# Performance work log

Hardware: AMD Instinct MI355X
Metric: run time of the kernel (lower is better)

The kernel has to match this reference:

```python
import jax, jax.numpy as jnp
import numpy as np

B, TQ, TK, D, H = 4, 2048, 2048, 512, 8
NEG = -1e9
LN_EPS = 1e-3  # Keras LayerNormalization default


def setup_inputs() -> dict:
    key = jax.random.key(0)
    ks = jax.random.split(key, 5)
    s = 0.02
    return {
        "queries": jax.random.normal(ks[0], (B, TQ, D), jnp.float32),
        "keys_in": jax.random.normal(ks[1], (B, TK, D), jnp.float32),
        "Wq": jax.random.normal(ks[2], (D, D), jnp.float32) * s,
        "bq": jnp.zeros((D,), jnp.float32),
        "Wk": jax.random.normal(ks[3], (D, D), jnp.float32) * s,
        "bk": jnp.zeros((D,), jnp.float32),
        "Wv": jax.random.normal(ks[4], (D, D), jnp.float32) * s,
        "bv": jnp.zeros((D,), jnp.float32),
        "gamma": jnp.ones((D,), jnp.float32),
        "beta": jnp.zeros((D,), jnp.float32),
    }


def reference(queries, keys_in, Wq, bq, Wk, bk, Wv, bv, gamma, beta):
    # Dense projections with relu activation (as in the original layer)
    Q = jax.nn.relu(queries @ Wq + bq)   # [B, Tq, D]
    K = jax.nn.relu(keys_in @ Wk + bk)   # [B, Tk, D]
    V = jax.nn.relu(keys_in @ Wv + bv)   # [B, Tk, D]

    b, tq, d = Q.shape
    tk = K.shape[1]
    dh = d // H
    # split_heads: tf.split(axis=-1)+concat(axis=0) == contiguous feature chunks per head
    Qh = Q.reshape(b, tq, H, dh)
    Kh = K.reshape(b, tk, H, dh)
    Vh = V.reshape(b, tk, H, dh)

    scores = jnp.einsum('bqhd,bkhd->bhqk', Qh, Kh) / jnp.sqrt(jnp.float32(dh))

    # key padding mask derived from per-head K content: sum(|K|) > 0 along dh
    kmask = jnp.sum(jnp.abs(Kh), axis=-1) > 0            # [B, Tk, H]
    kmask = jnp.transpose(kmask, (0, 2, 1))              # [B, H, Tk]
    scores = jnp.where(kmask[:, :, None, :], scores, NEG)

    attn = jax.nn.softmax(scores, axis=-1)               # [B, H, Tq, Tk]

    # query mask: zero out attention rows for all-zero query positions
    qmask = (jnp.sum(jnp.abs(Qh), axis=-1) > 0).astype(attn.dtype)  # [B, Tq, H]
    qmask = jnp.transpose(qmask, (0, 2, 1))              # [B, H, Tq]
    attn = attn * qmask[:, :, :, None]

    out = jnp.einsum('bhqk,bkhd->bqhd', attn, Vh).reshape(b, tq, d)

    # residual + LayerNorm (Keras default: last axis, eps=1e-3)
    res = out + queries
    mu = jnp.mean(res, axis=-1, keepdims=True)
    var = jnp.var(res, axis=-1, keepdims=True)
    return (res - mu) * jax.lax.rsqrt(var + LN_EPS) * gamma + beta
```

## Files before the change

### kernel.cpp

```cpp
#include <hip/hip_runtime.h>
#include <cstdint>

#define BB 4
#define TT 2048
#define DD 512
#define HH 8
#define DH 64
#define NT (TT / 64)
#define LOG2E 1.4426950408889634f

using bf16x8 = __attribute__((ext_vector_type(8))) __bf16;
using f32x4  = __attribute__((ext_vector_type(4))) float;
using f32x16 = __attribute__((ext_vector_type(16))) float;
using us8    = __attribute__((ext_vector_type(8))) unsigned short;
using us4    = __attribute__((ext_vector_type(4))) unsigned short;
using u32x2  = __attribute__((ext_vector_type(2))) unsigned int;

typedef const __attribute__((address_space(1))) unsigned int* as1cp;
typedef __attribute__((address_space(3))) unsigned int* as3p;

__device__ __forceinline__ void gload16(const void* g, void* l) {
  __builtin_amdgcn_global_load_lds((as1cp)(uintptr_t)g,
                                   (as3p)(unsigned int)(uintptr_t)l, 16, 0, 0);
}

__device__ __forceinline__ unsigned short f2bf(float x) {
  unsigned int u = __float_as_uint(x);
  u += 0x7fffu + ((u >> 16) & 1u);
  return (unsigned short)(u >> 16);
}
__device__ __forceinline__ float bf2f(unsigned short u) {
  return __uint_as_float(((unsigned int)u) << 16);
}
__device__ __forceinline__ f32x4 MFMA(bf16x8 a, bf16x8 b, f32x4 c) {
  return __builtin_amdgcn_mfma_f32_16x16x32_bf16(a, b, c, 0, 0, 0);
}
__device__ __forceinline__ f32x16 MFMA32(bf16x8 a, bf16x8 b, f32x16 c) {
  return __builtin_amdgcn_mfma_f32_32x32x16_bf16(a, b, c, 0, 0, 0);
}

#define WAITVM(N) asm volatile("s_waitcnt vmcnt(" #N ")" ::: "memory")
#define RAWBAR() asm volatile("s_barrier" ::: "memory")

__global__ __launch_bounds__(256) void prep_kernel(const float4* __restrict__ q,
                                                   const float4* __restrict__ k,
                                                   us4* __restrict__ qb,
                                                   us4* __restrict__ kb,
                                                   const float* __restrict__ Wq,
                                                   const float* __restrict__ Wk,
                                                   const float* __restrict__ Wv,
                                                   unsigned short* __restrict__ Wt) {
  __shared__ float tile[32][33];
  int id = blockIdx.x;
  if (id < 4096) {
    size_t i = (size_t)id * 256 + threadIdx.x;
    float4 a = q[i];
    us4 o; o[0] = f2bf(a.x); o[1] = f2bf(a.y); o[2] = f2bf(a.z); o[3] = f2bf(a.w);
    qb[i] = o;
    float4 b = k[i];
    us4 p; p[0] = f2bf(b.x); p[1] = f2bf(b.y); p[2] = f2bf(b.z); p[3] = f2bf(b.w);
    kb[i] = p;
  } else {
    int id2 = id - 4096;
    int z = id2 >> 8, rem = id2 & 255;
    const float* W = (z == 0) ? Wq : (z == 1) ? Wk : Wv;
    int k0 = (rem & 15) * 32, n0 = (rem >> 4) * 32;
    int r = threadIdx.x >> 5, c = threadIdx.x & 31;
#pragma unroll
    for (int p = 0; p < 4; ++p)
      tile[r + p * 8][c] = W[(size_t)(k0 + r + p * 8) * DD + n0 + c];
    __syncthreads();
    unsigned short* o = Wt + (size_t)z * DD * DD;
#pragma unroll
    for (int p = 0; p < 4; ++p)
      o[(size_t)(n0 + r + p * 8) * DD + k0 + c] = f2bf(tile[c][r + p * 8]);
  }
}

#define GSTAGE(kt2, pbuf)                                                    \
  {                                                                          \
    int t_ = threadIdx.x;                                                    \
    _Pragma("unroll")                                                        \
    for (int it_ = 0; it_ < 2; ++it_) {                                      \
      int c_ = t_ + it_ * 256;                                               \
      gload16(A  + (size_t)(mb + (c_ >> 2)) * DD + (kt2) * 32 + (c_ & 3) * 8,\
              &As[pbuf][(size_t)c_ * 8]);                                    \
      gload16(Bt + (size_t)(nb + (c_ >> 2)) * DD + (kt2) * 32 + (c_ & 3) * 8,\
              &Bs[pbuf][(size_t)c_ * 8]);                                    \
    }                                                                        \
  }

__global__ __launch_bounds__(256) void gemm_proj(const unsigned short* __restrict__ qb,
                                                 const unsigned short* __restrict__ kb,
                                                 const unsigned short* __restrict__ Wt,
                                                 const float* __restrict__ bq,
                                                 const float* __restrict__ bk,
                                                 const float* __restrict__ bv,
                                                 unsigned short* __restrict__ Qp,
                                                 unsigned short* __restrict__ Kp,
                                                 unsigned short* __restrict__ Vp) {
  int z = blockIdx.z;
  const unsigned short* A  = (z == 0) ? qb : kb;
  const unsigned short* Bt = Wt + (size_t)z * DD * DD;
  const float* bias = (z == 0) ? bq : (z == 1) ? bk : bv;
  unsigned short* out = (z == 0) ? Qp : (z == 1) ? Kp : Vp;
  const float osc = (z == 0) ? 0.125f * LOG2E : 1.0f;

  __shared__ __align__(16) unsigned short As[2][128 * 32];
  __shared__ __align__(16) unsigned short Bs[2][128 * 32];

  int mb = blockIdx.x * 128, nb = blockIdx.y * 128;
  int w = threadIdx.x >> 6, lane = threadIdx.x & 63;
  int l15 = lane & 15, lg = lane >> 4;
  int wr = (w >> 1) * 64, wc = (w & 1) * 64;

  f32x4 acc[4][4] = {};

  GSTAGE(0, 0);
  for (int kt = 0; kt < DD / 32; ++kt) {
    int pb2 = kt & 1;
    if (kt + 1 < DD / 32) {
      GSTAGE(kt + 1, pb2 ^ 1);
      WAITVM(4);
    } else {
      WAITVM(0);
    }
    RAWBAR();

    bf16x8 af[4], bf[4];
#pragma unroll
    for (int m = 0; m < 4; ++m)
      af[m] = *(const bf16x8*)&As[pb2][(wr + m * 16 + l15) * 32 + lg * 8];
#pragma unroll
    for (int n = 0; n < 4; ++n)
      bf[n] = *(const bf16x8*)&Bs[pb2][(wc + n * 16 + l15) * 32 + lg * 8];
#pragma unroll
    for (int m = 0; m < 4; ++m)
#pragma unroll
      for (int n = 0; n < 4; ++n)
        acc[m][n] = MFMA(af[m], bf[n], acc[m][n]);

    if (kt + 1 < DD / 32) RAWBAR();
  }

#pragma unroll
  for (int m = 0; m < 4; ++m)
#pragma unroll
    for (int n = 0; n < 4; ++n)
#pragma unroll
      for (int i = 0; i < 4; ++i) {
        int row = mb + wr + m * 16 + lg * 4 + i;
        int col = nb + wc + n * 16 + l15;
        float v = acc[m][n][i] + bias[col];
        out[(size_t)row * DD + col] = f2bf(fmaxf(v, 0.f) * osc);
      }
}

__global__ __launch_bounds__(256) void post_proj(const unsigned short* __restrict__ Qp,
                                                 const unsigned short* __restrict__ Kp,
                                                 const unsigned short* __restrict__ Vp,
                                                 unsigned short* __restrict__ Vt,
                                                 float* __restrict__ qmask,
                                                 uint2* __restrict__ kbits) {
  __shared__ unsigned short tile[64][72];
  int id = blockIdx.x;
  if (id < 1024) {
    int b = id >> 8, k0 = (id & 31) * 64, d0 = ((id >> 5) & 7) * 64;
    int t = threadIdx.x;
    int r = t >> 3, c8 = (t & 7) * 8;
#pragma unroll
    for (int p = 0; p < 2; ++p) {
      int row = r + p * 32;
      us8 v = *(const us8*)&Vp[(size_t)(b * TT + k0 + row) * DD + d0 + c8];
#pragma unroll
      for (int j = 0; j < 8; ++j) tile[row][c8 + j] = v[j];
    }
    __syncthreads();
#pragma unroll
    for (int p = 0; p < 2; ++p) {
      int dr = r + p * 32;
      us8 o;
#pragma unroll
      for (int j = 0; j < 8; ++j) o[j] = tile[c8 + j][dr];
      *(us8*)&Vt[((size_t)b * DD + d0 + dr) * TT + k0 + c8] = o;
    }
  } else {
    int wid = (id - 1024) * 4 + (threadIdx.x >> 6);
    int lane = threadIdx.x & 63;
    int side = wid >> 10;
    int rem = wid & 1023;
    int bh = rem >> 5, tl = rem & 31;
    int b = bh >> 3, h = bh & 7;
    const unsigned short* src =
        (side ? Kp : Qp) + ((size_t)(b * TT + tl * 64 + lane)) * DD + h * DH;
    float s = 0.f;
#pragma unroll
    for (int j = 0; j < 64; j += 8) {
      us8 v = *(const us8*)(src + j);
#pragma unroll
      for (int e = 0; e < 8; ++e) s += bf2f(v[e]);
    }
    if (side == 0) {
      qmask[(size_t)bh * TT + tl * 64 + lane] = (s > 0.f) ? 1.f : 0.f;
    } else {
      unsigned long long mb = __ballot(s > 0.f);
      if (lane == 0)
        kbits[bh * NT + tl] = make_uint2((unsigned int)mb, (unsigned int)(mb >> 32));
    }
  }
}

#define STAGE(tt, pbuf)                                                      \
  {                                                                          \
    int c0_ = threadIdx.x;                                                   \
    _Pragma("unroll")                                                        \
    for (int it_ = 0; it_ < 2; ++it_) {                                      \
      int c_ = c0_ + it_ * 256;                                              \
      int r_ = c_ >> 3, j_ = c_ & 7;                                         \
      int js_ = j_ ^ (r_ & 7);                                               \
      int kr_ = (r_ & ~12) | ((r_ & 4) << 1) | ((r_ & 8) >> 1);              \
      gload16(kg + (size_t)((tt) * 64 + kr_) * DD + js_ * 8,                 \
              &KsBuf[pbuf][(size_t)c_ * 8]);                                 \
      gload16(vg + (size_t)r_ * TT + (tt) * 64 + js_ * 8,                    \
              &VsBuf[pbuf][(size_t)c_ * 8]);                                 \
    }                                                                        \
  }

__global__ __launch_bounds__(256) void attn_kernel(
    const unsigned short* __restrict__ Qp,
    const unsigned short* __restrict__ Kp,
    const unsigned short* __restrict__ Vt,
    const uint2* __restrict__ kbits,
    const float* __restrict__ qmask,
    float* __restrict__ O) {
  __shared__ __align__(16) unsigned short KsBuf[2][64 * 64];
  __shared__ __align__(16) unsigned short VsBuf[2][64 * 64];

  const int w = threadIdx.x >> 6;
  const int lane = threadIdx.x & 63;
  const int l31 = lane & 31, h2 = lane >> 5;

  int flat = blockIdx.x;
  int wg = (flat & 7) * 64 + (flat >> 3);
  int qt = wg & 15, bh = wg >> 4;
  int h = bh & 7, b = bh >> 3;
  int q0 = qt * 128 + w * 32;

  const unsigned short* qbase =
      Qp + ((size_t)(b * TT + q0 + l31)) * DD + h * DH + h2 * 8;
  bf16x8 qf[4];
#pragma unroll
  for (int kd = 0; kd < 4; ++kd) qf[kd] = *(const bf16x8*)(qbase + kd * 16);

  const unsigned short* kg = Kp + ((size_t)b * TT) * DD + h * DH;
  const unsigned short* vg = Vt + ((size_t)(b * DD + h * DH)) * TT;
  const uint2* kb_ptr = kbits + (size_t)bh * NT;

  f32x16 oat0 = {}, oat1 = {};
  float m_i = -1e30f, l_i = 0.f;

  STAGE(0, 0);

  for (int t = 0; t < NT; ++t) {
    int pb = t & 1;
    if (t + 1 < NT) {
      STAGE(t + 1, pb ^ 1);
      WAITVM(4);
    } else {
      WAITVM(0);
    }
    RAWBAR();

    const unsigned short* ksb = &KsBuf[pb][0];
    const unsigned short* vsb = &VsBuf[pb][0];

    bf16x8 kf0[4], kf1[4], vf0[4], vf1[4];
#pragma unroll
    for (int kd = 0; kd < 4; ++kd) {
      int x = ((kd * 2 + h2) ^ (l31 & 7)) << 3;
      kf0[kd] = *(const bf16x8*)&ksb[l31 * 64 + x];
      kf1[kd] = *(const bf16x8*)&ksb[(32 + l31) * 64 + x];
      vf0[kd] = *(const bf16x8*)&vsb[l31 * 64 + x];
      vf1[kd] = *(const bf16x8*)&vsb[(32 + l31) * 64 + x];
    }

    f32x16 s0 = {}, s1 = {};
    __builtin_amdgcn_s_setprio(1);
#pragma unroll
    for (int kd = 0; kd < 4; ++kd) s0 = MFMA32(kf0[kd], qf[kd], s0);
#pragma unroll
    for (int kd = 0; kd < 4; ++kd) s1 = MFMA32(kf1[kd], qf[kd], s1);
    __builtin_amdgcn_s_setprio(0);

    uint2 kw = kb_ptr[t];
    if ((kw.x & kw.y) != 0xffffffffu) {
#pragma unroll
      for (int r = 0; r < 16; ++r) {
        int sh = ((r >> 3) << 4) + (h2 << 3) + (r & 7);
        if (!((kw.x >> sh) & 1)) s0[r] = -1e30f;
        if (!((kw.y >> sh) & 1)) s1[r] = -1e30f;
      }
    }

    float x0 = fmaxf(fmaxf(fmaxf(s0[0], s0[1]), fmaxf(s0[2], s0[3])),
                     fmaxf(fmaxf(s0[4], s0[5]), fmaxf(s0[6], s0[7])));
    float x1 = fmaxf(fmaxf(fmaxf(s0[8], s0[9]), fmaxf(s0[10], s0[11])),
                     fmaxf(fmaxf(s0[12], s0[13]), fmaxf(s0[14], s0[15])));
    float x2 = fmaxf(fmaxf(fmaxf(s1[0], s1[1]), fmaxf(s1[2], s1[3])),
                     fmaxf(fmaxf(s1[4], s1[5]), fmaxf(s1[6], s1[7])));
    float x3 = fmaxf(fmaxf(fmaxf(s1[8], s1[9]), fmaxf(s1[10], s1[11])),
                     fmaxf(fmaxf(s1[12], s1[13]), fmaxf(s1[14], s1[15])));
    float pm = fmaxf(fmaxf(x0, x1), fmaxf(x2, x3));
    u32x2 sw = __builtin_amdgcn_permlane32_swap(__float_as_uint(pm),
                                                __float_as_uint(pm), false, false);
    pm = fmaxf(__uint_as_float(sw[0]), __uint_as_float(sw[1]));

    if (__any(pm > m_i + 12.f)) {
      float mn = fmaxf(m_i, pm);
      float al = exp2f(m_i - mn);
      m_i = mn;
      l_i *= al;
#pragma unroll
      for (int r = 0; r < 16; ++r) { oat0[r] *= al; oat1[r] *= al; }
    }

    float a0 = 0.f, a1 = 0.f, a2 = 0.f, a3 = 0.f;
#pragma unroll
    for (int r = 0; r < 8; ++r)  { float p = exp2f(s0[r] - m_i); s0[r] = p; a0 += p; }
#pragma unroll
    for (int r = 8; r < 16; ++r) { float p = exp2f(s0[r] - m_i); s0[r] = p; a1 += p; }
#pragma unroll
    for (int r = 0; r < 8; ++r)  { float p = exp2f(s1[r] - m_i); s1[r] = p; a2 += p; }
#pragma unroll
    for (int r = 8; r < 16; ++r) { float p = exp2f(s1[r] - m_i); s1[r] = p; a3 += p; }
    float rs = (a0 + a1) + (a2 + a3);
    u32x2 sr = __builtin_amdgcn_permlane32_swap(__float_as_uint(rs),
                                                __float_as_uint(rs), false, false);
    rs = __uint_as_float(sr[0]) + __uint_as_float(sr[1]);
    l_i += rs;

    bf16x8 pbf[4];
#pragma unroll
    for (int j = 0; j < 8; ++j) {
      pbf[0][j] = (__bf16)s0[j];
      pbf[1][j] = (__bf16)s0[8 + j];
      pbf[2][j] = (__bf16)s1[j];
      pbf[3][j] = (__bf16)s1[8 + j];
    }

    __builtin_amdgcn_s_setprio(1);
#pragma unroll
    for (int ks = 0; ks < 4; ++ks) {
      oat0 = MFMA32(vf0[ks], pbf[ks], oat0);
      oat1 = MFMA32(vf1[ks], pbf[ks], oat1);
    }
    __builtin_amdgcn_s_setprio(0);

    if (t + 1 < NT) RAWBAR();
  }

  float qm = qmask[(size_t)bh * TT + q0 + l31];
  float sc = qm / fmaxf(l_i, 1e-30f);
  float* ob = O + ((size_t)(b * TT + q0 + l31)) * DD + h * DH + h2 * 4;
#pragma unroll
  for (int qq = 0; qq < 4; ++qq) {
    float4 v0 = make_float4(oat0[4 * qq + 0] * sc, oat0[4 * qq + 1] * sc,
                            oat0[4 * qq + 2] * sc, oat0[4 * qq + 3] * sc);
    *(float4*)(ob + 8 * qq) = v0;
    float4 v1 = make_float4(oat1[4 * qq + 0] * sc, oat1[4 * qq + 1] * sc,
                            oat1[4 * qq + 2] * sc, oat1[4 * qq + 3] * sc);
    *(float4*)(ob + 32 + 8 * qq) = v1;
  }
}

__global__ __launch_bounds__(256) void ln_kernel(const float* __restrict__ O,
                                                 const float* __restrict__ qin,
                                                 const float* __restrict__ gamma,
                                                 const float* __restrict__ beta,
                                                 float* __restrict__ out) {
  int row = blockIdx.x * 4 + (threadIdx.x >> 6);
  int lane = threadIdx.x & 63;
  size_t base = (size_t)row * DD + lane * 8;
  const float4* o4 = (const float4*)(O + base);
  const float4* q4 = (const float4*)(qin + base);
  float4 a = o4[0], b2 = o4[1], c = q4[0], d2 = q4[1];
  float v[8];
  v[0] = a.x + c.x; v[1] = a.y + c.y; v[2] = a.z + c.z; v[3] = a.w + c.w;
  v[4] = b2.x + d2.x; v[5] = b2.y + d2.y; v[6] = b2.z + d2.z; v[7] = b2.w + d2.w;
  float s = 0.f, s2 = 0.f;
#pragma unroll
  for (int j = 0; j < 8; ++j) { s += v[j]; s2 += v[j] * v[j]; }
#pragma unroll
  for (int xm = 1; xm < 64; xm <<= 1) {
    s += __shfl_xor(s, xm);
    s2 += __shfl_xor(s2, xm);
  }
  float mu = s * (1.0f / DD);
  float var = s2 * (1.0f / DD) - mu * mu;
  float rs = rsqrtf(var + 1e-3f);
  const float* g = gamma + lane * 8;
  const float* bb = beta + lane * 8;
  float* ob = out + base;
#pragma unroll
  for (int j = 0; j < 8; ++j) ob[j] = (v[j] - mu) * rs * g[j] + bb[j];
}

extern "C" void kernel_launch(void* const* d_in, const int* in_sizes, int n_in,
                              void* d_out, int out_size, void* d_ws, size_t ws_size,
                              hipStream_t stream) {
  (void)in_sizes; (void)n_in; (void)out_size; (void)ws_size;
  const float* queries = (const float*)d_in[0];
  const float* keys_in = (const float*)d_in[1];
  const float* Wq = (const float*)d_in[2];
  const float* bq = (const float*)d_in[3];
  const float* Wk = (const float*)d_in[4];
  const float* bk = (const float*)d_in[5];
  const float* Wv = (const float*)d_in[6];
  const float* bv = (const float*)d_in[7];
  const float* gamma = (const float*)d_in[8];
  const float* beta  = (const float*)d_in[9];
  float* out = (float*)d_out;

  char* ws = (char*)d_ws;
  unsigned short* qb = (unsigned short*)(ws);
  unsigned short* kb = (unsigned short*)(ws + (8ull << 20));
  float*          O  = (float*)(ws);
  unsigned short* Qp = (unsigned short*)(ws + (16ull << 20));
  unsigned short* Kp = (unsigned short*)(ws + (24ull << 20));
  unsigned short* Vp = (unsigned short*)(ws + (32ull << 20));
  unsigned short* Vt = (unsigned short*)(ws + (40ull << 20));
  unsigned short* Wt = (unsigned short*)(ws + (48ull << 20));
  float* qmaskp = (float*)(ws + (50ull << 20));
  uint2* kbitsp = (uint2*)(ws + (50ull << 20) + (512ull << 10));

  prep_kernel<<<4864, 256, 0, stream>>>((const float4*)queries, (const float4*)keys_in,
                                        (us4*)qb, (us4*)kb, Wq, Wk, Wv, Wt);
  gemm_proj<<<dim3(64, 4, 3), 256, 0, stream>>>(qb, kb, Wt, bq, bk, bv, Qp, Kp, Vp);
  post_proj<<<1536, 256, 0, stream>>>(Qp, Kp, Vp, Vt, qmaskp, kbitsp);
  attn_kernel<<<512, 256, 0, stream>>>(Qp, Kp, Vt, kbitsp, qmaskp, O);
  ln_kernel<<<2048, 256, 0, stream>>>(O, queries, gamma, beta, out);
}
```

Before: 203.0 us.

## Pre-pack K/V into MFMA fragment order and load directly to registers

post_proj now writes K and V into per-tile layouts that already match the MFMA operand fragments. This lets the attention kernel drop its LDS staging, barriers and async global-to-LDS copies, and instead software-pipeline K fragments in registers with coalesced 16-byte global loads. The attention output is also stored as bf16 rather than fp32, which shrinks the write and the LayerNorm read. In exchange, the four waves in a block no longer share K/V through LDS, so each wave fetches its own copy from global memory or L2. The bf16 output also loses precision before the residual add.

```diff
diff --git a/kernel.cpp b/kernel.cpp
--- a/kernel.cpp
+++ b/kernel.cpp
@@ -159,34 +159,52 @@
 __global__ __launch_bounds__(256) void post_proj(const unsigned short* __restrict__ Qp,
                                                  const unsigned short* __restrict__ Kp,
                                                  const unsigned short* __restrict__ Vp,
-                                                 unsigned short* __restrict__ Vt,
+                                                 unsigned short* __restrict__ Kpack,
+                                                 unsigned short* __restrict__ Vpack,
                                                  float* __restrict__ qmask,
                                                  uint2* __restrict__ kbits) {
-  __shared__ unsigned short tile[64][72];
+  __shared__ __align__(16) unsigned short tile[64 * 256];
   int id = blockIdx.x;
-  if (id < 1024) {
-    int b = id >> 8, k0 = (id & 31) * 64, d0 = ((id >> 5) & 7) * 64;
-    int t = threadIdx.x;
-    int r = t >> 3, c8 = (t & 7) * 8;
-#pragma unroll
-    for (int p = 0; p < 2; ++p) {
-      int row = r + p * 32;
-      us8 v = *(const us8*)&Vp[(size_t)(b * TT + k0 + row) * DD + d0 + c8];
-#pragma unroll
-      for (int j = 0; j < 8; ++j) tile[row][c8 + j] = v[j];
+  int w = threadIdx.x >> 6, lane = threadIdx.x & 63;
+  int l31 = lane & 31, h2 = lane >> 5;
+
+  if (id < 256) {
+    int b = id >> 6, t = (id >> 1) & 31, hg = id & 1;
+    {
+      int c0 = threadIdx.x;
+#pragma unroll
+      for (int it = 0; it < 8; ++it) {
+        int c = c0 + it * 256;
+        int row = c >> 5, ch = c & 31;
+        gload16(Vp + ((size_t)(b * TT + t * 64 + row)) * DD + hg * 256 + ch * 8,
+                tile + (size_t)c * 8);
+      }
     }
     __syncthreads();
 #pragma unroll
-    for (int p = 0; p < 2; ++p) {
-      int dr = r + p * 32;
+    for (int cc = 0; cc < 8; ++cc) {
+      int chunk = w * 8 + cc;
+      int hh = chunk >> 3, half = (cc >> 2) & 1, ks = cc & 3;
       us8 o;
 #pragma unroll
-      for (int j = 0; j < 8; ++j) o[j] = tile[c8 + j][dr];
-      *(us8*)&Vt[((size_t)b * DD + d0 + dr) * TT + k0 + c8] = o;
-    }
+      for (int j = 0; j < 8; ++j)
+        o[j] = tile[(ks * 16 + h2 * 8 + j) * 256 + hh * 64 + half * 32 + l31];
+      int bh = b * 8 + hg * 4 + hh;
+      *(us8*)(Vpack + ((((size_t)bh * NT + t) * 2 + half) * 4 + ks) * 512 + lane * 8) = o;
+    }
+  } else if (id < 768) {
+    int wid = (id - 256) * 4 + w;
+    int n = wid & 1, t = (wid >> 1) & 31, bh = wid >> 6;
+    int b = bh >> 3, h = bh & 7;
+    int bs = (l31 & ~12) | ((l31 & 4) << 1) | ((l31 & 8) >> 1);
+    const unsigned short* src =
+        Kp + ((size_t)(b * TT + t * 64 + 32 * n + bs)) * DD + h * DH + h2 * 8;
+    unsigned short* dst = Kpack + (((size_t)bh * NT + t) * 2 + n) * 2048 + lane * 8;
+#pragma unroll
+    for (int kd = 0; kd < 4; ++kd)
+      *(us8*)(dst + kd * 512) = *(const us8*)(src + kd * 16);
   } else {
-    int wid = (id - 1024) * 4 + (threadIdx.x >> 6);
-    int lane = threadIdx.x & 63;
+    int wid = (id - 768) * 4 + w;
     int side = wid >> 10;
     int rem = wid & 1023;
     int bh = rem >> 5, tl = rem & 31;
@@ -210,32 +228,101 @@
   }
 }
 
-#define STAGE(tt, pbuf)                                                      \
-  {                                                                          \
-    int c0_ = threadIdx.x;                                                   \
-    _Pragma("unroll")                                                        \
-    for (int it_ = 0; it_ < 2; ++it_) {                                      \
-      int c_ = c0_ + it_ * 256;                                              \
-      int r_ = c_ >> 3, j_ = c_ & 7;                                         \
-      int js_ = j_ ^ (r_ & 7);                                               \
-      int kr_ = (r_ & ~12) | ((r_ & 4) << 1) | ((r_ & 8) >> 1);              \
-      gload16(kg + (size_t)((tt) * 64 + kr_) * DD + js_ * 8,                 \
-              &KsBuf[pbuf][(size_t)c_ * 8]);                                 \
-      gload16(vg + (size_t)r_ * TT + (tt) * 64 + js_ * 8,                    \
-              &VsBuf[pbuf][(size_t)c_ * 8]);                                 \
-    }                                                                        \
-  }
+__device__ __forceinline__ void attn_body(
+    int t, int tp,
+    const bf16x8 (&Kc)[8], bf16x8 (&Kn)[8], const bf16x8 (&qf)[4],
+    f32x16& oat0, f32x16& oat1, float& m_i, float& l_i,
+    const unsigned short* __restrict__ kgp, const unsigned short* __restrict__ vgp,
+    const uint2* __restrict__ kb_ptr, int h2) {
+  f32x16 s0 = {}, s1 = {};
+  __builtin_amdgcn_s_setprio(1);
+#pragma unroll
+  for (int kd = 0; kd < 4; ++kd) s0 = MFMA32(Kc[kd], qf[kd], s0);
+#pragma unroll
+  for (int kd = 0; kd < 4; ++kd) s1 = MFMA32(Kc[4 + kd], qf[kd], s1);
+  __builtin_amdgcn_s_setprio(0);
+
+  const unsigned short* kn = kgp + (size_t)tp * 4096;
+#pragma unroll
+  for (int c = 0; c < 8; ++c) Kn[c] = *(const bf16x8*)(kn + c * 512);
+
+  bf16x8 vc[8];
+  const unsigned short* vp = vgp + (size_t)t * 4096;
+#pragma unroll
+  for (int c = 0; c < 8; ++c) vc[c] = *(const bf16x8*)(vp + c * 512);
+
+  uint2 kw = kb_ptr[t];
+  if ((kw.x & kw.y) != 0xffffffffu) {
+#pragma unroll
+    for (int r = 0; r < 16; ++r) {
+      int sh = ((r >> 3) << 4) + (h2 << 3) + (r & 7);
+      if (!((kw.x >> sh) & 1)) s0[r] = -1e30f;
+      if (!((kw.y >> sh) & 1)) s1[r] = -1e30f;
+    }
+  }
+
+  float x0 = fmaxf(fmaxf(fmaxf(s0[0], s0[1]), fmaxf(s0[2], s0[3])),
+                   fmaxf(fmaxf(s0[4], s0[5]), fmaxf(s0[6], s0[7])));
+  float x1 = fmaxf(fmaxf(fmaxf(s0[8], s0[9]), fmaxf(s0[10], s0[11])),
+                   fmaxf(fmaxf(s0[12], s0[13]), fmaxf(s0[14], s0[15])));
+  float x2 = fmaxf(fmaxf(fmaxf(s1[0], s1[1]), fmaxf(s1[2], s1[3])),
+                   fmaxf(fmaxf(s1[4], s1[5]), fmaxf(s1[6], s1[7])));
+  float x3 = fmaxf(fmaxf(fmaxf(s1[8], s1[9]), fmaxf(s1[10], s1[11])),
+                   fmaxf(fmaxf(s1[12], s1[13]), fmaxf(s1[14], s1[15])));
+  float pm = fmaxf(fmaxf(x0, x1), fmaxf(x2, x3));
+  u32x2 sw = __builtin_amdgcn_permlane32_swap(__float_as_uint(pm),
+                                              __float_as_uint(pm), false, false);
+  pm = fmaxf(__uint_as_float(sw[0]), __uint_as_float(sw[1]));
+
+  if (__any(pm > m_i + 12.f)) {
+    float mn = fmaxf(m_i, pm);
+    float al = exp2f(m_i - mn);
+    m_i = mn;
+    l_i *= al;
+#pragma unroll
+    for (int r = 0; r < 16; ++r) { oat0[r] *= al; oat1[r] *= al; }
+  }
+
+  float a0 = 0.f, a1 = 0.f, a2 = 0.f, a3 = 0.f;
+#pragma unroll
+  for (int r = 0; r < 8; ++r)  { float p = exp2f(s0[r] - m_i); s0[r] = p; a0 += p; }
+#pragma unroll
+  for (int r = 8; r < 16; ++r) { float p = exp2f(s0[r] - m_i); s0[r] = p; a1 += p; }
+#pragma unroll
+  for (int r = 0; r < 8; ++r)  { float p = exp2f(s1[r] - m_i); s1[r] = p; a2 += p; }
+#pragma unroll
+  for (int r = 8; r < 16; ++r) { float p = exp2f(s1[r] - m_i); s1[r] = p; a3 += p; }
+  float rs = (a0 + a1) + (a2 + a3);
+  u32x2 sr = __builtin_amdgcn_permlane32_swap(__float_as_uint(rs),
+                                              __float_as_uint(rs), false, false);
+  rs = __uint_as_float(sr[0]) + __uint_as_float(sr[1]);
+  l_i += rs;
+
+  bf16x8 pbf[4];
+#pragma unroll
+  for (int j = 0; j < 8; ++j) {
+    pbf[0][j] = (__bf16)s0[j];
+    pbf[1][j] = (__bf16)s0[8 + j];
+    pbf[2][j] = (__bf16)s1[j];
+    pbf[3][j] = (__bf16)s1[8 + j];
+  }
+
+  __builtin_amdgcn_s_setprio(1);
+#pragma unroll
+  for (int ks = 0; ks < 4; ++ks) {
+    oat0 = MFMA32(vc[ks], pbf[ks], oat0);
+    oat1 = MFMA32(vc[4 + ks], pbf[ks], oat1);
+  }
+  __builtin_amdgcn_s_setprio(0);
+}
 
 __global__ __launch_bounds__(256) void attn_kernel(
     const unsigned short* __restrict__ Qp,
-    const unsigned short* __restrict__ Kp,
-    const unsigned short* __restrict__ Vt,
+    const unsigned short* __restrict__ Kpack,
+    const unsigned short* __restrict__ Vpack,
     const uint2* __restrict__ kbits,
     const float* __restrict__ qmask,
-    float* __restrict__ O) {
-  __shared__ __align__(16) unsigned short KsBuf[2][64 * 64];
-  __shared__ __align__(16) unsigned short VsBuf[2][64 * 64];
-
+    unsigned short* __restrict__ O) {
   const int w = threadIdx.x >> 6;
   const int lane = threadIdx.x & 63;
   const int l31 = lane & 31, h2 = lane >> 5;
@@ -252,128 +339,40 @@
 #pragma unroll
   for (int kd = 0; kd < 4; ++kd) qf[kd] = *(const bf16x8*)(qbase + kd * 16);
 
-  const unsigned short* kg = Kp + ((size_t)b * TT) * DD + h * DH;
-  const unsigned short* vg = Vt + ((size_t)(b * DD + h * DH)) * TT;
+  const unsigned short* kgp = Kpack + (size_t)bh * NT * 4096 + lane * 8;
+  const unsigned short* vgp = Vpack + (size_t)bh * NT * 4096 + lane * 8;
   const uint2* kb_ptr = kbits + (size_t)bh * NT;
 
   f32x16 oat0 = {}, oat1 = {};
   float m_i = -1e30f, l_i = 0.f;
 
-  STAGE(0, 0);
-
-  for (int t = 0; t < NT; ++t) {
-    int pb = t & 1;
-    if (t + 1 < NT) {
-      STAGE(t + 1, pb ^ 1);
-      WAITVM(4);
-    } else {
-      WAITVM(0);
-    }
-    RAWBAR();
-
-    const unsigned short* ksb = &KsBuf[pb][0];
-    const unsigned short* vsb = &VsBuf[pb][0];
-
-    bf16x8 kf0[4], kf1[4], vf0[4], vf1[4];
-#pragma unroll
-    for (int kd = 0; kd < 4; ++kd) {
-      int x = ((kd * 2 + h2) ^ (l31 & 7)) << 3;
-      kf0[kd] = *(const bf16x8*)&ksb[l31 * 64 + x];
-      kf1[kd] = *(const bf16x8*)&ksb[(32 + l31) * 64 + x];
-      vf0[kd] = *(const bf16x8*)&vsb[l31 * 64 + x];
-      vf1[kd] = *(const bf16x8*)&vsb[(32 + l31) * 64 + x];
-    }
-
-    f32x16 s0 = {}, s1 = {};
-    __builtin_amdgcn_s_setprio(1);
-#pragma unroll
-    for (int kd = 0; kd < 4; ++kd) s0 = MFMA32(kf0[kd], qf[kd], s0);
-#pragma unroll
-    for (int kd = 0; kd < 4; ++kd) s1 = MFMA32(kf1[kd], qf[kd], s1);
-    __builtin_amdgcn_s_setprio(0);
-
-    uint2 kw = kb_ptr[t];
-    if ((kw.x & kw.y) != 0xffffffffu) {
-#pragma unroll
-      for (int r = 0; r < 16; ++r) {
-        int sh = ((r >> 3) << 4) + (h2 << 3) + (r & 7);
-        if (!((kw.x >> sh) & 1)) s0[r] = -1e30f;
-        if (!((kw.y >> sh) & 1)) s1[r] = -1e30f;
-      }
-    }
-
-    float x0 = fmaxf(fmaxf(fmaxf(s0[0], s0[1]), fmaxf(s0[2], s0[3])),
-                     fmaxf(fmaxf(s0[4], s0[5]), fmaxf(s0[6], s0[7])));
-    float x1 = fmaxf(fmaxf(fmaxf(s0[8], s0[9]), fmaxf(s0[10], s0[11])),
-                     fmaxf(fmaxf(s0[12], s0[13]), fmaxf(s0[14], s0[15])));
-    float x2 = fmaxf(fmaxf(fmaxf(s1[0], s1[1]), fmaxf(s1[2], s1[3])),
-                     fmaxf(fmaxf(s1[4], s1[5]), fmaxf(s1[6], s1[7])));
-    float x3 = fmaxf(fmaxf(fmaxf(s1[8], s1[9]), fmaxf(s1[10], s1[11])),
-                     fmaxf(fmaxf(s1[12], s1[13]), fmaxf(s1[14], s1[15])));
-    float pm = fmaxf(fmaxf(x0, x1), fmaxf(x2, x3));
-    u32x2 sw = __builtin_amdgcn_permlane32_swap(__float_as_uint(pm),
-                                                __float_as_uint(pm), false, false);
-    pm = fmaxf(__uint_as_float(sw[0]), __uint_as_float(sw[1]));
-
-    if (__any(pm > m_i + 12.f)) {
-      float mn = fmaxf(m_i, pm);
-      float al = exp2f(m_i - mn);
-      m_i = mn;
-      l_i *= al;
-#pragma unroll
-      for (int r = 0; r < 16; ++r) { oat0[r] *= al; oat1[r] *= al; }
-    }
-
-    float a0 = 0.f, a1 = 0.f, a2 = 0.f, a3 = 0.f;
-#pragma unroll
-    for (int r = 0; r < 8; ++r)  { float p = exp2f(s0[r] - m_i); s0[r] = p; a0 += p; }
-#pragma unroll
-    for (int r = 8; r < 16; ++r) { float p = exp2f(s0[r] - m_i); s0[r] = p; a1 += p; }
-#pragma unroll
-    for (int r = 0; r < 8; ++r)  { float p = exp2f(s1[r] - m_i); s1[r] = p; a2 += p; }
-#pragma unroll
-    for (int r = 8; r < 16; ++r) { float p = exp2f(s1[r] - m_i); s1[r] = p; a3 += p; }
-    float rs = (a0 + a1) + (a2 + a3);
-    u32x2 sr = __builtin_amdgcn_permlane32_swap(__float_as_uint(rs),
-                                                __float_as_uint(rs), false, false);
-    rs = __uint_as_float(sr[0]) + __uint_as_float(sr[1]);
-    l_i += rs;
-
-    bf16x8 pbf[4];
-#pragma unroll
-    for (int j = 0; j < 8; ++j) {
-      pbf[0][j] = (__bf16)s0[j];
-      pbf[1][j] = (__bf16)s0[8 + j];
-      pbf[2][j] = (__bf16)s1[j];
-      pbf[3][j] = (__bf16)s1[8 + j];
-    }
-
-    __builtin_amdgcn_s_setprio(1);
-#pragma unroll
-    for (int ks = 0; ks < 4; ++ks) {
-      oat0 = MFMA32(vf0[ks], pbf[ks], oat0);
-      oat1 = MFMA32(vf1[ks], pbf[ks], oat1);
-    }
-    __builtin_amdgcn_s_setprio(0);
-
-    if (t + 1 < NT) RAWBAR();
+  bf16x8 kA[8], kB[8];
+#pragma unroll
+  for (int c = 0; c < 8; ++c) kA[c] = *(const bf16x8*)(kgp + c * 512);
+
+  for (int t = 0; t < NT; t += 2) {
+    attn_body(t, t + 1, kA, kB, qf, oat0, oat1, m_i, l_i, kgp, vgp, kb_ptr, h2);
+    attn_body(t + 1, (t + 2 < NT) ? t + 2 : 0, kB, kA, qf, oat0, oat1, m_i, l_i,
+              kgp, vgp, kb_ptr, h2);
   }
 
   float qm = qmask[(size_t)bh * TT + q0 + l31];
   float sc = qm / fmaxf(l_i, 1e-30f);
-  float* ob = O + ((size_t)(b * TT + q0 + l31)) * DD + h * DH + h2 * 4;
+  unsigned short* ob = O + ((size_t)(b * TT + q0 + l31)) * DD + h * DH + h2 * 4;
 #pragma unroll
   for (int qq = 0; qq < 4; ++qq) {
-    float4 v0 = make_float4(oat0[4 * qq + 0] * sc, oat0[4 * qq + 1] * sc,
-                            oat0[4 * qq + 2] * sc, oat0[4 * qq + 3] * sc);
-    *(float4*)(ob + 8 * qq) = v0;
-    float4 v1 = make_float4(oat1[4 * qq + 0] * sc, oat1[4 * qq + 1] * sc,
-                            oat1[4 * qq + 2] * sc, oat1[4 * qq + 3] * sc);
-    *(float4*)(ob + 32 + 8 * qq) = v1;
-  }
-}
-
-__global__ __launch_bounds__(256) void ln_kernel(const float* __restrict__ O,
+    us4 w0, w1;
+#pragma unroll
+    for (int i = 0; i < 4; ++i) {
+      w0[i] = f2bf(oat0[4 * qq + i] * sc);
+      w1[i] = f2bf(oat1[4 * qq + i] * sc);
+    }
+    *(us4*)(ob + 8 * qq) = w0;
+    *(us4*)(ob + 32 + 8 * qq) = w1;
+  }
+}
+
+__global__ __launch_bounds__(256) void ln_kernel(const unsigned short* __restrict__ O,
                                                  const float* __restrict__ qin,
                                                  const float* __restrict__ gamma,
                                                  const float* __restrict__ beta,
@@ -381,12 +380,13 @@
   int row = blockIdx.x * 4 + (threadIdx.x >> 6);
   int lane = threadIdx.x & 63;
   size_t base = (size_t)row * DD + lane * 8;
-  const float4* o4 = (const float4*)(O + base);
+  us8 o = *(const us8*)(O + base);
   const float4* q4 = (const float4*)(qin + base);
-  float4 a = o4[0], b2 = o4[1], c = q4[0], d2 = q4[1];
+  float4 c = q4[0], d2 = q4[1];
+  float qv[8] = {c.x, c.y, c.z, c.w, d2.x, d2.y, d2.z, d2.w};
   float v[8];
-  v[0] = a.x + c.x; v[1] = a.y + c.y; v[2] = a.z + c.z; v[3] = a.w + c.w;
-  v[4] = b2.x + d2.x; v[5] = b2.y + d2.y; v[6] = b2.z + d2.z; v[7] = b2.w + d2.w;
+#pragma unroll
+  for (int j = 0; j < 8; ++j) v[j] = bf2f(o[j]) + qv[j];
   float s = 0.f, s2 = 0.f;
 #pragma unroll
   for (int j = 0; j < 8; ++j) { s += v[j]; s2 += v[j] * v[j]; }
@@ -424,11 +424,12 @@
   char* ws = (char*)d_ws;
   unsigned short* qb = (unsigned short*)(ws);
   unsigned short* kb = (unsigned short*)(ws + (8ull << 20));
-  float*          O  = (float*)(ws);
+  unsigned short* Obf   = (unsigned short*)(ws);
+  unsigned short* Vpack = (unsigned short*)(ws + (8ull << 20));
   unsigned short* Qp = (unsigned short*)(ws + (16ull << 20));
   unsigned short* Kp = (unsigned short*)(ws + (24ull << 20));
   unsigned short* Vp = (unsigned short*)(ws + (32ull << 20));
-  unsigned short* Vt = (unsigned short*)(ws + (40ull << 20));
+  unsigned short* Kpack = (unsigned short*)(ws + (40ull << 20));
   unsigned short* Wt = (unsigned short*)(ws + (48ull << 20));
   float* qmaskp = (float*)(ws + (50ull << 20));
   uint2* kbitsp = (uint2*)(ws + (50ull << 20) + (512ull << 10));
@@ -436,7 +437,7 @@
   prep_kernel<<<4864, 256, 0, stream>>>((const float4*)queries, (const float4*)keys_in,
                                         (us4*)qb, (us4*)kb, Wq, Wk, Wv, Wt);
   gemm_proj<<<dim3(64, 4, 3), 256, 0, stream>>>(qb, kb, Wt, bq, bk, bv, Qp, Kp, Vp);
-  post_proj<<<1536, 256, 0, stream>>>(Qp, Kp, Vp, Vt, qmaskp, kbitsp);
-  attn_kernel<<<512, 256, 0, stream>>>(Qp, Kp, Vt, kbitsp, qmaskp, O);
-  ln_kernel<<<2048, 256, 0, stream>>>(O, queries, gamma, beta, out);
-}
+  post_proj<<<1280, 256, 0, stream>>>(Qp, Kp, Vp, Kpack, Vpack, qmaskp, kbitsp);
+  attn_kernel<<<512, 256, 0, stream>>>(Qp, Kpack, Vpack, kbitsp, qmaskp, Obf);
+  ln_kernel<<<2048, 256, 0, stream>>>(Obf, queries, gamma, beta, out);
+}
```

Result: faster. 192.8 us (-5.0%).
